# Optimization experiments

Measured on AMD Instinct MI355X. Metric: run time of the kernel, lower is better.

Reference implementation:

```python
import jax, jax.numpy as jnp
import numpy as np

EMBED_DIM = 1024
NUM_HEADS = 16
HEAD_DIM = EMBED_DIM // NUM_HEADS
SCALE_BASE = EMBED_DIM  # XPOS(head_dim, embed_dim): embed_dim is scale_base
BSZ, SEQ = 8, 1024


def xpos_apply(x, downscale):
    # x: [B*H, L, D]; standard xpos (torchscale) rotary with position-dependent scale
    L, D = x.shape[1], x.shape[2]
    half = D // 2
    s = (jnp.arange(0, D, 2, dtype=jnp.float32) + 0.4 * D) / (1.4 * D)  # [half]
    min_pos = -(L // 2)  # offset = 0
    pos = jnp.arange(min_pos, min_pos + L, dtype=jnp.float32)  # [L]
    scale = s[None, :] ** (pos[:, None] / SCALE_BASE)  # [L, half]
    inv_freq = 1.0 / (10000.0 ** (jnp.arange(half, dtype=jnp.float32) / half))
    sinus = jnp.arange(L, dtype=jnp.float32)[:, None] * inv_freq[None, :]  # [L, half]
    sin, cos = jnp.sin(sinus), jnp.cos(sinus)
    if downscale:
        scale = 1.0 / scale
    # duplicate_interleave: repeat each column twice -> [L, D]
    sin_d = jnp.repeat(sin * scale, 2, axis=-1)
    cos_d = jnp.repeat(cos * scale, 2, axis=-1)
    x1, x2 = x[..., 0::2], x[..., 1::2]
    rot = jnp.stack([-x2, x1], axis=-1).reshape(x.shape)  # rotate_every_two
    return x * cos_d + rot * sin_d


def setup_inputs() -> dict:
    key = jax.random.key(0)
    ks = jax.random.split(key, 12)
    std = 0.02
    inp = {
        'query': jax.random.normal(ks[0], (BSZ, SEQ, EMBED_DIM), jnp.float32),
        'key': jax.random.normal(ks[1], (BSZ, SEQ, EMBED_DIM), jnp.float32),
        'value': jax.random.normal(ks[2], (BSZ, SEQ, EMBED_DIM), jnp.float32),
        'wq': jax.random.normal(ks[3], (EMBED_DIM, EMBED_DIM), jnp.float32) * std,
        'bq': jax.random.normal(ks[4], (EMBED_DIM,), jnp.float32) * std,
        'wk': jax.random.normal(ks[5], (EMBED_DIM, EMBED_DIM), jnp.float32) * std,
        'bk': jax.random.normal(ks[6], (EMBED_DIM,), jnp.float32) * std,
        'wv': jax.random.normal(ks[7], (EMBED_DIM, EMBED_DIM), jnp.float32) * std,
        'bv': jax.random.normal(ks[8], (EMBED_DIM,), jnp.float32) * std,
        'wo': jax.random.normal(ks[9], (EMBED_DIM, EMBED_DIM), jnp.float32) * std,
        'bo': jax.random.normal(ks[10], (EMBED_DIM,), jnp.float32) * std,
    }
    return inp


def reference(query, key, value, wq, bq, wk, bk, wv, bv, wo, bo):
    B, T, E = query.shape
    S = key.shape[1]
    scaling = HEAD_DIM ** -0.5
    q = (query @ wq.T + bq) * scaling
    k = key @ wk.T + bk
    v = value @ wv.T + bv

    def split_heads(x, L):
        return x.reshape(B, L, NUM_HEADS, HEAD_DIM).transpose(0, 2, 1, 3).reshape(B * NUM_HEADS, L, HEAD_DIM)

    q = split_heads(q, T)
    k = split_heads(k, S)
    v = split_heads(v, S)
    k = xpos_apply(k, downscale=True)
    q = xpos_apply(q, downscale=False)
    attn_w = jnp.einsum('btd,bsd->bts', q, k)  # [B*H, T, S]
    attn_w = jax.nn.softmax(attn_w.astype(jnp.float32), axis=-1).astype(q.dtype)
    attn = jnp.einsum('bts,bsd->btd', attn_w, v)  # [B*H, T, D]
    attn = attn.reshape(B, NUM_HEADS, T, HEAD_DIM).transpose(0, 2, 1, 3).reshape(B, T, E)
    return attn @ wo.T + bo
```

## Files before the change

kernel.cpp:

```cpp
#include <hip/hip_runtime.h>


#define BSZ  8
#define SEQ  1024
#define EMB  1024
#define NH   16
#define HD   64
#define HALF 32
#define BH   (BSZ*NH)
#define MROWS (BSZ*SEQ)

typedef __attribute__((ext_vector_type(4))) float f32x4;
typedef __attribute__((ext_vector_type(8))) short bf16x8;
typedef __attribute__((ext_vector_type(8))) unsigned short u16x8;

__device__ __forceinline__ ushort f2bf(float f) {
    union { float f; unsigned u; } v; v.f = f;
    return (ushort)((v.u + 0x7FFFu + ((v.u >> 16) & 1u)) >> 16);
}

__device__ __forceinline__ void async16(void* lds, const void* g) {
    __builtin_amdgcn_global_load_lds(
        (const __attribute__((address_space(1))) unsigned int*)g,
        (__attribute__((address_space(3))) unsigned int*)lds, 16, 0, 0);
}

__global__ __launch_bounds__(256)
void castw_kernel(const float* __restrict__ w0, const float* __restrict__ w1,
                  const float* __restrict__ w2, const float* __restrict__ w3,
                  ushort* __restrict__ d0, ushort* __restrict__ d1,
                  ushort* __restrict__ d2, ushort* __restrict__ d3, int n4) {
    int i = blockIdx.x * 256 + threadIdx.x;
    if (i >= n4) return;
    const float* s = blockIdx.y == 0 ? w0 : blockIdx.y == 1 ? w1
                   : blockIdx.y == 2 ? w2 : w3;
    ushort* d = blockIdx.y == 0 ? d0 : blockIdx.y == 1 ? d1
              : blockIdx.y == 2 ? d2 : d3;
    float4 v = reinterpret_cast<const float4*>(s)[i];
    ushort4 o;
    o.x = f2bf(v.x); o.y = f2bf(v.y); o.z = f2bf(v.z); o.w = f2bf(v.w);
    reinterpret_cast<ushort4*>(d)[i] = o;
}

__global__ __launch_bounds__(256)
void xpos_tables_kernel(float* __restrict__ tab) {
    int idx = blockIdx.x * 256 + threadIdx.x;
    if (idx >= SEQ * HALF) return;
    int t = idx >> 5;
    int j = idx & 31;
    float s        = (2.0f * (float)j + 0.4f * (float)HD) / (1.4f * (float)HD);
    float pos      = (float)(t - SEQ / 2);
    float scale    = powf(s, pos * (1.0f / 1024.0f));
    float inv_freq = powf(10000.0f, -(float)j / (float)HALF);
    float ang      = (float)t * inv_freq;
    float sn = sinf(ang), cs = cosf(ang);
    float inv_scale = 1.0f / scale;
    tab[0 * SEQ * HALF + idx] = sn * scale;
    tab[1 * SEQ * HALF + idx] = cs * scale;
    tab[2 * SEQ * HALF + idx] = sn * inv_scale;
    tab[3 * SEQ * HALF + idx] = cs * inv_scale;
}

__global__ __launch_bounds__(256)
void qkv_gemm_kernel(const float* __restrict__ Aq, const float* __restrict__ Ak,
                     const float* __restrict__ Av,
                     const ushort* __restrict__ Wq, const ushort* __restrict__ Wk,
                     const ushort* __restrict__ Wv,
                     const float* __restrict__ bq, const float* __restrict__ bk,
                     const float* __restrict__ bv,
                     const float* __restrict__ tab,
                     ushort* __restrict__ oq, ushort* __restrict__ ok,
                     ushort* __restrict__ ov) {
    __shared__ ushort As[128 * 64];
    __shared__ ushort Bs[128 * 64];
    const int ymode = blockIdx.y;
    const float*  A    = ymode == 0 ? Aq : ymode == 1 ? Ak : Av;
    const ushort* W    = ymode == 0 ? Wq : ymode == 1 ? Wk : Wv;
    const float*  bias = ymode == 0 ? bq : ymode == 1 ? bk : bv;
    ushort*       outp = ymode == 0 ? oq : ymode == 1 ? ok : ov;

    const int tid  = threadIdx.x;
    const int lane = tid & 63;
    const int w    = tid >> 6;
    const int g    = lane >> 4;
    const int c    = lane & 15;
    const int wr   = w >> 1, wc = w & 1;

    int lid = blockIdx.x;
    int wg  = (lid & 7) * 64 + (lid >> 3);
    const int row0 = (wg >> 3) * 128;
    const int col0 = (wg & 7) * 128;

    f32x4 acc[4][4] = {};

    const int ar  = tid >> 1;
    const int ach = (tid & 1) * 32;
    const int asw = (ar & 7) << 4;

    int srow[4], scol[4];
    #pragma unroll
    for (int i = 0; i < 4; ++i) {
        int f = i * 4096 + tid * 16;
        int r = f >> 7, cb = f & 127;
        srow[i] = r;
        scol[i] = (cb ^ ((r & 7) << 4)) >> 1;
    }

    for (int k0 = 0; k0 < EMB; k0 += 64) {
        const float4* asrc = reinterpret_cast<const float4*>(
            &A[(size_t)(row0 + ar) * EMB + k0 + ach]);
        float4 av[8];
        #pragma unroll
        for (int i = 0; i < 8; ++i) av[i] = asrc[i];
        #pragma unroll
        for (int a = 0; a < 4; ++a) {
            u16x8 u;
            const float* pf = reinterpret_cast<const float*>(&av[2 * a]);
            #pragma unroll
            for (int e = 0; e < 8; ++e) u[e] = f2bf(pf[e]);
            int byt = ar * 128 + ((2 * (ach + 8 * a)) ^ asw);
            *reinterpret_cast<u16x8*>(reinterpret_cast<char*>(As) + byt) = u;
        }
        #pragma unroll
        for (int i = 0; i < 4; ++i)
            async16(&Bs[i * 2048 + w * 512],
                    &W[(size_t)(col0 + srow[i]) * EMB + k0 + scol[i]]);
        __syncthreads();

        #pragma unroll
        for (int ks = 0; ks < 2; ++ks) {
            bf16x8 af[4], bfr[4];
            #pragma unroll
            for (int mi = 0; mi < 4; ++mi) {
                int r = wr * 64 + mi * 16 + c;
                int byt = r * 128 + ((ks * 64 + g * 16) ^ ((r & 7) << 4));
                af[mi] = *reinterpret_cast<const bf16x8*>(
                    reinterpret_cast<const char*>(As) + byt);
            }
            #pragma unroll
            for (int ni = 0; ni < 4; ++ni) {
                int r = wc * 64 + ni * 16 + c;
                int byt = r * 128 + ((ks * 64 + g * 16) ^ ((r & 7) << 4));
                bfr[ni] = *reinterpret_cast<const bf16x8*>(
                    reinterpret_cast<const char*>(Bs) + byt);
            }
            #pragma unroll
            for (int mi = 0; mi < 4; ++mi)
                #pragma unroll
                for (int ni = 0; ni < 4; ++ni)
                    acc[mi][ni] = __builtin_amdgcn_mfma_f32_16x16x32_bf16(
                        af[mi], bfr[ni], acc[mi][ni], 0, 0, 0);
        }
        __syncthreads();
    }

    #pragma unroll
    for (int ni = 0; ni < 4; ++ni) {
        int n = col0 + wc * 64 + ni * 16 + c;
        float bn = bias[n];
        #pragma unroll
        for (int mi = 0; mi < 4; ++mi) {
            #pragma unroll
            for (int r = 0; r < 4; ++r) {
                int m = row0 + wr * 64 + mi * 16 + g * 4 + r;
                float val = acc[mi][ni][r] + bn;
                if (ymode == 0) val *= 0.125f;
                if (ymode != 2) {
                    int t = m & (SEQ - 1);
                    int d = n & 63;
                    const int base = (ymode == 0 ? 0 : 2) * SEQ * HALF + t * HALF;
                    float sn = tab[base + (d >> 1)];
                    float cs = tab[base + SEQ * HALF + (d >> 1)];
                    float other = __shfl_xor(val, 1);
                    val = val * cs + ((d & 1) ? other * sn : -other * sn);
                }
                int b = m >> 10, t = m & 1023;
                int h = n >> 6,  d = n & 63;
                outp[(((size_t)b * NH + h) * SEQ + t) * HD + d] = f2bf(val);
            }
        }
    }
}

__global__ __launch_bounds__(256)
void vtrans_kernel(const ushort* __restrict__ v, ushort* __restrict__ vt) {
    __shared__ ushort T[64][72];
    const int tid = threadIdx.x;
    const int bh  = blockIdx.y;
    const int t0  = blockIdx.x * 64;
    const ushort* vb = &v[((size_t)bh * SEQ + t0) * HD];
    #pragma unroll
    for (int p = 0; p < 2; ++p) {
        int chunk = p * 256 + tid;
        int tl = chunk >> 3;
        int d8 = (chunk & 7) * 8;
        ushort tmp[8];
        *reinterpret_cast<uint4*>(tmp) =
            *reinterpret_cast<const uint4*>(&vb[tl * HD + d8]);
        #pragma unroll
        for (int j = 0; j < 8; ++j) T[d8 + j][tl] = tmp[j];
    }
    __syncthreads();
    ushort* ob = &vt[(size_t)bh * HD * SEQ + t0];
    #pragma unroll
    for (int p = 0; p < 2; ++p) {
        int chunk = p * 256 + tid;
        int dl = chunk >> 3;
        int t8 = (chunk & 7) * 8;
        *reinterpret_cast<uint4*>(&ob[(size_t)dl * SEQ + t8]) =
            *reinterpret_cast<const uint4*>(&T[dl][t8]);
    }
}

__global__ __launch_bounds__(256)
void attn_kernel(const ushort* __restrict__ qg, const ushort* __restrict__ kg,
                 const ushort* __restrict__ vtg, ushort* __restrict__ og) {
    __shared__ ushort Ks[2 * 4096];
    __shared__ ushort Vs[2 * 4096];
    __shared__ ushort Ps[4096];
    const int tid  = threadIdx.x;
    const int lane = tid & 63;
    const int w    = tid >> 6;
    const int g    = lane >> 4;
    const int c    = lane & 15;

    int lid = blockIdx.x;
    int wg  = (lid & 7) * 256 + (lid >> 3);
    const int bh = wg >> 4;
    const int q0 = (wg & 15) * 64;

    const ushort* qrow = &qg[((size_t)bh * SEQ + q0 + w * 16 + c) * HD];
    bf16x8 qf[2];
    qf[0] = *reinterpret_cast<const bf16x8*>(qrow + g * 8);
    qf[1] = *reinterpret_cast<const bf16x8*>(qrow + 32 + g * 8);

    float m_run[4], l_part[4];
    f32x4 oacc[4] = {};
    #pragma unroll
    for (int r = 0; r < 4; ++r) { m_run[r] = -1e30f; l_part[r] = 0.f; }

    int srow[2], scol[2];
    #pragma unroll
    for (int i = 0; i < 2; ++i) {
        int f = i * 4096 + tid * 16;
        int r = f >> 7, cb = f & 127;
        srow[i] = r; scol[i] = (cb ^ ((r & 7) << 4)) >> 1;
    }

    const ushort* kb  = &kg[(size_t)bh * SEQ * HD];
    const ushort* vtb = &vtg[(size_t)bh * HD * SEQ];

    auto stage = [&](int buf, int kt) {
        #pragma unroll
        for (int i = 0; i < 2; ++i) {
            async16(&Ks[buf * 4096 + i * 2048 + w * 512],
                    &kb[(size_t)(kt + srow[i]) * HD + scol[i]]);
            async16(&Vs[buf * 4096 + i * 2048 + w * 512],
                    &vtb[(size_t)srow[i] * SEQ + kt + scol[i]]);
        }
    };

    stage(0, 0);
    __syncthreads();

    char* pbase = reinterpret_cast<char*>(Ps) + w * 2048;

    for (int kt = 0; kt < SEQ; kt += 64) {
        const int cur = (kt >> 6) & 1;
        if (kt + 64 < SEQ) stage(cur ^ 1, kt + 64);

        const char* kbase = reinterpret_cast<const char*>(Ks) + cur * 8192;
        const char* vbase = reinterpret_cast<const char*>(Vs) + cur * 8192;

        f32x4 s[4];
        #pragma unroll
        for (int j = 0; j < 4; ++j) {
            int key = j * 16 + c;
            int sw  = (key & 7) << 4;
            f32x4 a = {};
            #pragma unroll
            for (int ks = 0; ks < 2; ++ks) {
                bf16x8 kf = *reinterpret_cast<const bf16x8*>(
                    kbase + key * 128 + ((ks * 64 + g * 16) ^ sw));
                a = __builtin_amdgcn_mfma_f32_16x16x32_bf16(qf[ks], kf, a, 0, 0, 0);
            }
            s[j] = a;
        }

        float pmax[4];
        #pragma unroll
        for (int r = 0; r < 4; ++r)
            pmax[r] = fmaxf(fmaxf(s[0][r], s[1][r]), fmaxf(s[2][r], s[3][r]));
        int need = (pmax[0] > m_run[0] + 8.f) || (pmax[1] > m_run[1] + 8.f) ||
                   (pmax[2] > m_run[2] + 8.f) || (pmax[3] > m_run[3] + 8.f);
        if (__any(need)) {
            #pragma unroll
            for (int r = 0; r < 4; ++r) {
                float mx = pmax[r];
                mx = fmaxf(mx, __shfl_xor(mx, 1));
                mx = fmaxf(mx, __shfl_xor(mx, 2));
                mx = fmaxf(mx, __shfl_xor(mx, 4));
                mx = fmaxf(mx, __shfl_xor(mx, 8));
                float mn = fmaxf(m_run[r], mx);
                float alpha = __expf(m_run[r] - mn);
                l_part[r] *= alpha;
                #pragma unroll
                for (int dblk = 0; dblk < 4; ++dblk) oacc[dblk][r] *= alpha;
                m_run[r] = mn;
            }
        }

        #pragma unroll
        for (int r = 0; r < 4; ++r) {
            int q  = g * 4 + r;
            int sw = (q & 7) << 4;
            #pragma unroll
            for (int j = 0; j < 4; ++j) {
                float p = __expf(s[j][r] - m_run[r]);
                l_part[r] += p;
                int byt = q * 128 + (((j * 16 + c) * 2) ^ sw);
                *reinterpret_cast<ushort*>(pbase + byt) = f2bf(p);
            }
        }

        #pragma unroll
        for (int ks = 0; ks < 2; ++ks) {
            bf16x8 pf = *reinterpret_cast<const bf16x8*>(
                pbase + c * 128 + ((ks * 64 + g * 16) ^ ((c & 7) << 4)));
            #pragma unroll
            for (int dblk = 0; dblk < 4; ++dblk) {
                int d = dblk * 16 + c;
                bf16x8 vf = *reinterpret_cast<const bf16x8*>(
                    vbase + d * 128 + ((ks * 64 + g * 16) ^ ((d & 7) << 4)));
                oacc[dblk] = __builtin_amdgcn_mfma_f32_16x16x32_bf16(
                    pf, vf, oacc[dblk], 0, 0, 0);
            }
        }
        __syncthreads();
    }

    #pragma unroll
    for (int r = 0; r < 4; ++r) {
        float rs = l_part[r];
        rs += __shfl_xor(rs, 1);
        rs += __shfl_xor(rs, 2);
        rs += __shfl_xor(rs, 4);
        rs += __shfl_xor(rs, 8);
        float inv = 1.f / rs;
        int q = q0 + w * 16 + g * 4 + r;
        #pragma unroll
        for (int dblk = 0; dblk < 4; ++dblk)
            og[((size_t)bh * SEQ + q) * HD + dblk * 16 + c] =
                f2bf(oacc[dblk][r] * inv);
    }
}

__global__ __launch_bounds__(256)
void outproj_kernel(const ushort* __restrict__ A, const ushort* __restrict__ W,
                    const float* __restrict__ bias, float* __restrict__ out) {
    __shared__ ushort As[128 * 64];
    __shared__ ushort Bs[128 * 64];
    const int tid  = threadIdx.x;
    const int lane = tid & 63;
    const int w    = tid >> 6;
    const int g    = lane >> 4;
    const int c    = lane & 15;
    const int wr   = w >> 1, wc = w & 1;

    int lid = blockIdx.x;
    int wg  = (lid & 7) * 64 + (lid >> 3);
    const int row0 = (wg >> 3) * 128;
    const int col0 = (wg & 7) * 128;

    f32x4 acc[4][4] = {};

    int srow[4], scol[4];
    #pragma unroll
    for (int i = 0; i < 4; ++i) {
        int f = i * 4096 + tid * 16;
        int r = f >> 7, cb = f & 127;
        srow[i] = r;
        scol[i] = (cb ^ ((r & 7) << 4)) >> 1;
    }

    for (int k0 = 0; k0 < EMB; k0 += 64) {
        int h = k0 >> 6;
        #pragma unroll
        for (int i = 0; i < 4; ++i)
            async16(&As[i * 2048 + w * 512],
                    &A[(((size_t)(row0 >> 10) * NH + h) * SEQ +
                        (row0 & 1023) + srow[i]) * HD + scol[i]]);
        #pragma unroll
        for (int i = 0; i < 4; ++i)
            async16(&Bs[i * 2048 + w * 512],
                    &W[(size_t)(col0 + srow[i]) * EMB + k0 + scol[i]]);
        __syncthreads();

        #pragma unroll
        for (int ks = 0; ks < 2; ++ks) {
            bf16x8 af[4], bfr[4];
            #pragma unroll
            for (int mi = 0; mi < 4; ++mi) {
                int r = wr * 64 + mi * 16 + c;
                int byt = r * 128 + ((ks * 64 + g * 16) ^ ((r & 7) << 4));
                af[mi] = *reinterpret_cast<const bf16x8*>(
                    reinterpret_cast<const char*>(As) + byt);
            }
            #pragma unroll
            for (int ni = 0; ni < 4; ++ni) {
                int r = wc * 64 + ni * 16 + c;
                int byt = r * 128 + ((ks * 64 + g * 16) ^ ((r & 7) << 4));
                bfr[ni] = *reinterpret_cast<const bf16x8*>(
                    reinterpret_cast<const char*>(Bs) + byt);
            }
            #pragma unroll
            for (int mi = 0; mi < 4; ++mi)
                #pragma unroll
                for (int ni = 0; ni < 4; ++ni)
                    acc[mi][ni] = __builtin_amdgcn_mfma_f32_16x16x32_bf16(
                        af[mi], bfr[ni], acc[mi][ni], 0, 0, 0);
        }
        __syncthreads();
    }

    #pragma unroll
    for (int ni = 0; ni < 4; ++ni) {
        int n = col0 + wc * 64 + ni * 16 + c;
        float bn = bias[n];
        #pragma unroll
        for (int mi = 0; mi < 4; ++mi) {
            #pragma unroll
            for (int r = 0; r < 4; ++r) {
                int m = row0 + wr * 64 + mi * 16 + g * 4 + r;
                out[(size_t)m * EMB + n] = acc[mi][ni][r] + bn;
            }
        }
    }
}

extern "C" void kernel_launch(void* const* d_in, const int* in_sizes, int n_in,
                              void* d_out, int out_size, void* d_ws,
                              size_t ws_size, hipStream_t stream) {
    const float* query = (const float*)d_in[0];
    const float* key_  = (const float*)d_in[1];
    const float* value = (const float*)d_in[2];
    const float* wq    = (const float*)d_in[3];
    const float* bq    = (const float*)d_in[4];
    const float* wk    = (const float*)d_in[5];
    const float* bk    = (const float*)d_in[6];
    const float* wv    = (const float*)d_in[7];
    const float* bv    = (const float*)d_in[8];
    const float* wo    = (const float*)d_in[9];
    const float* bo    = (const float*)d_in[10];

    ushort* ws16 = (ushort*)d_ws;
    const size_t NX = (size_t)MROWS * EMB;
    const size_t NW = (size_t)EMB * EMB;
    ushort* qb  = ws16;
    ushort* kb  = qb + NX;
    ushort* vb  = kb + NX;
    ushort* vt  = vb + NX;
    ushort* wqb = vt + NX;
    ushort* wkb = wqb + NW;
    ushort* wvb = wkb + NW;
    ushort* wob = wvb + NW;
    float*  tab = (float*)(wob + NW);

    const int nw4 = (int)(NW / 4);
    castw_kernel<<<dim3(nw4 / 256, 4), 256, 0, stream>>>(
        wq, wk, wv, wo, wqb, wkb, wvb, wob, nw4);
    xpos_tables_kernel<<<SEQ * HALF / 256, 256, 0, stream>>>(tab);

    qkv_gemm_kernel<<<dim3(512, 3), 256, 0, stream>>>(
        query, key_, value, wqb, wkb, wvb, bq, bk, bv, tab, qb, kb, vb);

    vtrans_kernel<<<dim3(16, 128), 256, 0, stream>>>(vb, vt);

    attn_kernel<<<2048, 256, 0, stream>>>(qb, kb, vt, vb);

    outproj_kernel<<<512, 256, 0, stream>>>(vb, wob, bo, (float*)d_out);
}
```

Before: 428.5 us.

## Double-buffer LDS in QKV and output GEMMs, use packed bf16 conversion

```diff
diff --git a/kernel.cpp b/kernel.cpp
--- a/kernel.cpp
+++ b/kernel.cpp
@@ -12,11 +12,16 @@
 
 typedef __attribute__((ext_vector_type(4))) float f32x4;
 typedef __attribute__((ext_vector_type(8))) short bf16x8;
-typedef __attribute__((ext_vector_type(8))) unsigned short u16x8;
 
 __device__ __forceinline__ ushort f2bf(float f) {
     union { float f; unsigned u; } v; v.f = f;
     return (ushort)((v.u + 0x7FFFu + ((v.u >> 16) & 1u)) >> 16);
+}
+
+__device__ __forceinline__ unsigned cvt_pk_bf16(float a, float b) {
+    unsigned r;
+    asm("v_cvt_pk_bf16_f32 %0, %1, %2" : "=v"(r) : "v"(a), "v"(b));
+    return r;
 }
 
 __device__ __forceinline__ void async16(void* lds, const void* g) {
@@ -71,8 +76,8 @@
                      const float* __restrict__ tab,
                      ushort* __restrict__ oq, ushort* __restrict__ ok,
                      ushort* __restrict__ ov) {
-    __shared__ ushort As[128 * 64];
-    __shared__ ushort Bs[128 * 64];
+    __shared__ ushort As[2][128 * 64];
+    __shared__ ushort Bs[2][128 * 64];
     const int ymode = blockIdx.y;
     const float*  A    = ymode == 0 ? Aq : ymode == 1 ? Ak : Av;
     const ushort* W    = ymode == 0 ? Wq : ymode == 1 ? Wk : Wv;
@@ -96,6 +101,8 @@
     const int ar  = tid >> 1;
     const int ach = (tid & 1) * 32;
     const int asw = (ar & 7) << 4;
+    const float4* abase4 =
+        reinterpret_cast<const float4*>(A + (size_t)(row0 + ar) * EMB) + (ach >> 2);
 
     int srow[4], scol[4];
     #pragma unroll
@@ -106,43 +113,58 @@
         scol[i] = (cb ^ ((r & 7) << 4)) >> 1;
     }
 
-    for (int k0 = 0; k0 < EMB; k0 += 64) {
-        const float4* asrc = reinterpret_cast<const float4*>(
-            &A[(size_t)(row0 + ar) * EMB + k0 + ach]);
-        float4 av[8];
-        #pragma unroll
-        for (int i = 0; i < 8; ++i) av[i] = asrc[i];
+    auto stageB = [&](int buf, int k0) {
+        #pragma unroll
+        for (int i = 0; i < 4; ++i)
+            async16(&Bs[buf][i * 2048 + w * 512],
+                    &W[(size_t)(col0 + srow[i]) * EMB + k0 + scol[i]]);
+    };
+    auto writeA = [&](int buf, const float4* av) {
         #pragma unroll
         for (int a = 0; a < 4; ++a) {
-            u16x8 u;
             const float* pf = reinterpret_cast<const float*>(&av[2 * a]);
-            #pragma unroll
-            for (int e = 0; e < 8; ++e) u[e] = f2bf(pf[e]);
-            int byt = ar * 128 + ((2 * (ach + 8 * a)) ^ asw);
-            *reinterpret_cast<u16x8*>(reinterpret_cast<char*>(As) + byt) = u;
-        }
-        #pragma unroll
-        for (int i = 0; i < 4; ++i)
-            async16(&Bs[i * 2048 + w * 512],
-                    &W[(size_t)(col0 + srow[i]) * EMB + k0 + scol[i]]);
-        __syncthreads();
-
+            uint4 u;
+            u.x = cvt_pk_bf16(pf[0], pf[1]);
+            u.y = cvt_pk_bf16(pf[2], pf[3]);
+            u.z = cvt_pk_bf16(pf[4], pf[5]);
+            u.w = cvt_pk_bf16(pf[6], pf[7]);
+            *reinterpret_cast<uint4*>(
+                reinterpret_cast<char*>(&As[buf][0]) + ar * 128 +
+                ((2 * (ach + 8 * a)) ^ asw)) = u;
+        }
+    };
+
+    float4 av[8];
+    #pragma unroll
+    for (int i = 0; i < 8; ++i) av[i] = abase4[i];
+    writeA(0, av);
+    stageB(0, 0);
+    __syncthreads();
+
+    for (int t = 0; t < 16; ++t) {
+        const int cur = t & 1;
+        if (t < 15) {
+            #pragma unroll
+            for (int i = 0; i < 8; ++i) av[i] = abase4[(t + 1) * 16 + i];
+            stageB(cur ^ 1, (t + 1) * 64);
+        }
+
+        const char* abase = reinterpret_cast<const char*>(&As[cur][0]);
+        const char* bbase = reinterpret_cast<const char*>(&Bs[cur][0]);
         #pragma unroll
         for (int ks = 0; ks < 2; ++ks) {
             bf16x8 af[4], bfr[4];
             #pragma unroll
             for (int mi = 0; mi < 4; ++mi) {
                 int r = wr * 64 + mi * 16 + c;
-                int byt = r * 128 + ((ks * 64 + g * 16) ^ ((r & 7) << 4));
                 af[mi] = *reinterpret_cast<const bf16x8*>(
-                    reinterpret_cast<const char*>(As) + byt);
+                    abase + r * 128 + ((ks * 64 + g * 16) ^ ((r & 7) << 4)));
             }
             #pragma unroll
             for (int ni = 0; ni < 4; ++ni) {
                 int r = wc * 64 + ni * 16 + c;
-                int byt = r * 128 + ((ks * 64 + g * 16) ^ ((r & 7) << 4));
                 bfr[ni] = *reinterpret_cast<const bf16x8*>(
-                    reinterpret_cast<const char*>(Bs) + byt);
+                    bbase + r * 128 + ((ks * 64 + g * 16) ^ ((r & 7) << 4)));
             }
             #pragma unroll
             for (int mi = 0; mi < 4; ++mi)
@@ -151,6 +173,8 @@
                     acc[mi][ni] = __builtin_amdgcn_mfma_f32_16x16x32_bf16(
                         af[mi], bfr[ni], acc[mi][ni], 0, 0, 0);
         }
+
+        if (t < 15) writeA(cur ^ 1, av);
         __syncthreads();
     }
 
@@ -174,9 +198,115 @@
                     float other = __shfl_xor(val, 1);
                     val = val * cs + ((d & 1) ? other * sn : -other * sn);
                 }
-                int b = m >> 10, t = m & 1023;
-                int h = n >> 6,  d = n & 63;
-                outp[(((size_t)b * NH + h) * SEQ + t) * HD + d] = f2bf(val);
+                int b = m >> 10, t2 = m & 1023;
+                int h = n >> 6,  d2 = n & 63;
+                outp[(((size_t)b * NH + h) * SEQ + t2) * HD + d2] = f2bf(val);
+            }
+        }
+    }
+}
+
+template <int MODE>
+__global__ __launch_bounds__(256)
+void gemm_bf16_kernel(const ushort* __restrict__ A, const ushort* __restrict__ W,
+                      const float* __restrict__ bias, const float* __restrict__ tab,
+                      void* __restrict__ outp) {
+    __shared__ ushort As[2][128 * 64];
+    __shared__ ushort Bs[2][128 * 64];
+    const int tid  = threadIdx.x;
+    const int lane = tid & 63;
+    const int w    = tid >> 6;
+    const int g    = lane >> 4;
+    const int c    = lane & 15;
+    const int wr   = w >> 1, wc = w & 1;
+
+    int lid = blockIdx.x;
+    int wg  = (lid & 7) * 64 + (lid >> 3);
+    const int row0 = (wg >> 3) * 128;
+    const int col0 = (wg & 7) * 128;
+
+    f32x4 acc[4][4] = {};
+
+    int srow[4], scol[4];
+    #pragma unroll
+    for (int i = 0; i < 4; ++i) {
+        int f = i * 4096 + tid * 16;
+        int r = f >> 7, cb = f & 127;
+        srow[i] = r;
+        scol[i] = (cb ^ ((r & 7) << 4)) >> 1;
+    }
+
+    auto stage = [&](int buf, int k0) {
+        #pragma unroll
+        for (int i = 0; i < 4; ++i) {
+            const ushort* srcA;
+            if (MODE == 3) {
+                int h = k0 >> 6;
+                srcA = &A[(((size_t)(row0 >> 10) * NH + h) * SEQ +
+                           (row0 & 1023) + srow[i]) * HD + scol[i]];
+            } else {
+                srcA = &A[(size_t)(row0 + srow[i]) * EMB + k0 + scol[i]];
+            }
+            async16(&As[buf][i * 2048 + w * 512], srcA);
+        }
+        #pragma unroll
+        for (int i = 0; i < 4; ++i)
+            async16(&Bs[buf][i * 2048 + w * 512],
+                    &W[(size_t)(col0 + srow[i]) * EMB + k0 + scol[i]]);
+    };
+
+    stage(0, 0);
+    __syncthreads();
+
+    for (int t = 0; t < 16; ++t) {
+        const int cur = t & 1;
+        if (t < 15) stage(cur ^ 1, (t + 1) * 64);
+
+        const char* abase = reinterpret_cast<const char*>(&As[cur][0]);
+        const char* bbase = reinterpret_cast<const char*>(&Bs[cur][0]);
+        #pragma unroll
+        for (int ks = 0; ks < 2; ++ks) {
+            bf16x8 af[4], bfr[4];
+            #pragma unroll
+            for (int mi = 0; mi < 4; ++mi) {
+                int r = wr * 64 + mi * 16 + c;
+                af[mi] = *reinterpret_cast<const bf16x8*>(
+                    abase + r * 128 + ((ks * 64 + g * 16) ^ ((r & 7) << 4)));
+            }
+            #pragma unroll
+            for (int ni = 0; ni < 4; ++ni) {
+                int r = wc * 64 + ni * 16 + c;
+                bfr[ni] = *reinterpret_cast<const bf16x8*>(
+                    bbase + r * 128 + ((ks * 64 + g * 16) ^ ((r & 7) << 4)));
+            }
+            #pragma unroll
+            for (int mi = 0; mi < 4; ++mi)
+                #pragma unroll
+                for (int ni = 0; ni < 4; ++ni)
+                    acc[mi][ni] = __builtin_amdgcn_mfma_f32_16x16x32_bf16(
+                        af[mi], bfr[ni], acc[mi][ni], 0, 0, 0);
+        }
+        __syncthreads();
+    }
+
+    #pragma unroll
+    for (int ni = 0; ni < 4; ++ni) {
+        int n = col0 + wc * 64 + ni * 16 + c;
+        float bn = bias[n];
+        #pragma unroll
+        for (int mi = 0; mi < 4; ++mi) {
+            #pragma unroll
+            for (int r = 0; r < 4; ++r) {
+                int m = row0 + wr * 64 + mi * 16 + g * 4 + r;
+                float val = acc[mi][ni][r] + bn;
+                if (MODE == 3) {
+                    ((float*)outp)[(size_t)m * EMB + n] = val;
+                } else {
+                    int b = m >> 10, t = m & 1023;
+                    int h = n >> 6,  d = n & 63;
+                    ((ushort*)outp)[(((size_t)b * NH + h) * SEQ + t) * HD + d] =
+                        f2bf(val);
+                }
             }
         }
     }
@@ -314,13 +444,18 @@
         for (int r = 0; r < 4; ++r) {
             int q  = g * 4 + r;
             int sw = (q & 7) << 4;
-            #pragma unroll
-            for (int j = 0; j < 4; ++j) {
-                float p = __expf(s[j][r] - m_run[r]);
-                l_part[r] += p;
-                int byt = q * 128 + (((j * 16 + c) * 2) ^ sw);
-                *reinterpret_cast<ushort*>(pbase + byt) = f2bf(p);
-            }
+            char* pq = pbase + q * 128;
+            float p0 = __expf(s[0][r] - m_run[r]);
+            float p1 = __expf(s[1][r] - m_run[r]);
+            float p2 = __expf(s[2][r] - m_run[r]);
+            float p3 = __expf(s[3][r] - m_run[r]);
+            l_part[r] += (p0 + p1) + (p2 + p3);
+            unsigned pk01 = cvt_pk_bf16(p0, p1);
+            unsigned pk23 = cvt_pk_bf16(p2, p3);
+            *reinterpret_cast<ushort*>(pq + (( 0 + 2 * c) ^ sw)) = (ushort)pk01;
+            *reinterpret_cast<ushort*>(pq + ((32 + 2 * c) ^ sw)) = (ushort)(pk01 >> 16);
+            *reinterpret_cast<ushort*>(pq + ((64 + 2 * c) ^ sw)) = (ushort)pk23;
+            *reinterpret_cast<ushort*>(pq + ((96 + 2 * c) ^ sw)) = (ushort)(pk23 >> 16);
         }
 
         #pragma unroll
@@ -352,89 +487,6 @@
         for (int dblk = 0; dblk < 4; ++dblk)
             og[((size_t)bh * SEQ + q) * HD + dblk * 16 + c] =
                 f2bf(oacc[dblk][r] * inv);
-    }
-}
-
-__global__ __launch_bounds__(256)
-void outproj_kernel(const ushort* __restrict__ A, const ushort* __restrict__ W,
-                    const float* __restrict__ bias, float* __restrict__ out) {
-    __shared__ ushort As[128 * 64];
-    __shared__ ushort Bs[128 * 64];
-    const int tid  = threadIdx.x;
-    const int lane = tid & 63;
-    const int w    = tid >> 6;
-    const int g    = lane >> 4;
-    const int c    = lane & 15;
-    const int wr   = w >> 1, wc = w & 1;
-
-    int lid = blockIdx.x;
-    int wg  = (lid & 7) * 64 + (lid >> 3);
-    const int row0 = (wg >> 3) * 128;
-    const int col0 = (wg & 7) * 128;
-
-    f32x4 acc[4][4] = {};
-
-    int srow[4], scol[4];
-    #pragma unroll
-    for (int i = 0; i < 4; ++i) {
-        int f = i * 4096 + tid * 16;
-        int r = f >> 7, cb = f & 127;
-        srow[i] = r;
-        scol[i] = (cb ^ ((r & 7) << 4)) >> 1;
-    }
-
-    for (int k0 = 0; k0 < EMB; k0 += 64) {
-        int h = k0 >> 6;
-        #pragma unroll
-        for (int i = 0; i < 4; ++i)
-            async16(&As[i * 2048 + w * 512],
-                    &A[(((size_t)(row0 >> 10) * NH + h) * SEQ +
-                        (row0 & 1023) + srow[i]) * HD + scol[i]]);
-        #pragma unroll
-        for (int i = 0; i < 4; ++i)
-            async16(&Bs[i * 2048 + w * 512],
-                    &W[(size_t)(col0 + srow[i]) * EMB + k0 + scol[i]]);
-        __syncthreads();
-
-        #pragma unroll
-        for (int ks = 0; ks < 2; ++ks) {
-            bf16x8 af[4], bfr[4];
-            #pragma unroll
-            for (int mi = 0; mi < 4; ++mi) {
-                int r = wr * 64 + mi * 16 + c;
-                int byt = r * 128 + ((ks * 64 + g * 16) ^ ((r & 7) << 4));
-                af[mi] = *reinterpret_cast<const bf16x8*>(
-                    reinterpret_cast<const char*>(As) + byt);
-            }
-            #pragma unroll
-            for (int ni = 0; ni < 4; ++ni) {
-                int r = wc * 64 + ni * 16 + c;
-                int byt = r * 128 + ((ks * 64 + g * 16) ^ ((r & 7) << 4));
-                bfr[ni] = *reinterpret_cast<const bf16x8*>(
-                    reinterpret_cast<const char*>(Bs) + byt);
-            }
-            #pragma unroll
-            for (int mi = 0; mi < 4; ++mi)
-                #pragma unroll
-                for (int ni = 0; ni < 4; ++ni)
-                    acc[mi][ni] = __builtin_amdgcn_mfma_f32_16x16x32_bf16(
-                        af[mi], bfr[ni], acc[mi][ni], 0, 0, 0);
-        }
-        __syncthreads();
-    }
-
-    #pragma unroll
-    for (int ni = 0; ni < 4; ++ni) {
-        int n = col0 + wc * 64 + ni * 16 + c;
-        float bn = bias[n];
-        #pragma unroll
-        for (int mi = 0; mi < 4; ++mi) {
-            #pragma unroll
-            for (int r = 0; r < 4; ++r) {
-                int m = row0 + wr * 64 + mi * 16 + g * 4 + r;
-                out[(size_t)m * EMB + n] = acc[mi][ni][r] + bn;
-            }
-        }
     }
 }
 
@@ -456,17 +508,19 @@
     ushort* ws16 = (ushort*)d_ws;
     const size_t NX = (size_t)MROWS * EMB;
     const size_t NW = (size_t)EMB * EMB;
-    ushort* qb  = ws16;
-    ushort* kb  = qb + NX;
-    ushort* vb  = kb + NX;
-    ushort* vt  = vb + NX;
-    ushort* wqb = vt + NX;
+    ushort* wqb = ws16;
     ushort* wkb = wqb + NW;
     ushort* wvb = wkb + NW;
     ushort* wob = wvb + NW;
     float*  tab = (float*)(wob + NW);
+    ushort* qb  = (ushort*)(tab + 4 * SEQ * HALF);
+    ushort* kb  = qb + NX;
+    ushort* vb  = kb + NX;
+    ushort* vt  = vb + NX;
+    ushort* ob  = vt + NX;
 
     const int nw4 = (int)(NW / 4);
+
     castw_kernel<<<dim3(nw4 / 256, 4), 256, 0, stream>>>(
         wq, wk, wv, wo, wqb, wkb, wvb, wob, nw4);
     xpos_tables_kernel<<<SEQ * HALF / 256, 256, 0, stream>>>(tab);
@@ -476,7 +530,8 @@
 
     vtrans_kernel<<<dim3(16, 128), 256, 0, stream>>>(vb, vt);
 
-    attn_kernel<<<2048, 256, 0, stream>>>(qb, kb, vt, vb);
-
-    outproj_kernel<<<512, 256, 0, stream>>>(vb, wob, bo, (float*)d_out);
-}
+    attn_kernel<<<2048, 256, 0, stream>>>(qb, kb, vt, ob);
+
+    gemm_bf16_kernel<3><<<512, 256, 0, stream>>>(ob, wob, bo, nullptr,
+                                                 (float*)d_out);
+}
```

Result: faster. 410.1 us (-4.3%).
